# Kernel optimization log

Hardware: AMD Instinct MI355X
Metric: run time of the kernel (lower is better)

Reference implementation:

```python
import jax, jax.numpy as jnp
import numpy as np

B, S, D = 8, 2048, 1024

def setup_inputs() -> dict:
    key = jax.random.key(0)
    ks = jax.random.split(key, 7)
    x = jax.random.normal(ks[0], (B, S, D), dtype=jnp.float32)
    s = 1.0 / np.sqrt(D)
    Wq = jax.random.normal(ks[1], (D, D), dtype=jnp.float32) * s
    bq = jax.random.normal(ks[2], (D,), dtype=jnp.float32) * 0.01
    Wk = jax.random.normal(ks[3], (D, D), dtype=jnp.float32) * s
    bk = jax.random.normal(ks[4], (D,), dtype=jnp.float32) * 0.01
    Wv = jax.random.normal(ks[5], (D, D), dtype=jnp.float32) * s
    bv = jax.random.normal(ks[6], (D,), dtype=jnp.float32) * 0.01
    return {"x": x, "Wq": Wq, "bq": bq, "Wk": Wk, "bk": bk, "Wv": Wv, "bv": bv}

def reference(x, Wq, bq, Wk, bk, Wv, bv):
    # QKV projections: [B,S,D]
    Q = jnp.einsum('bsd,de->bse', x, Wq) + bq
    K = jnp.einsum('bsd,de->bse', x, Wk) + bk
    V = jnp.einsum('bsd,de->bse', x, Wv) + bv
    scale = 1.0 / jnp.sqrt(jnp.asarray(Q.shape[-1], Q.dtype))
    attn = jnp.einsum('bqd,bkd->bqk', Q, K) * scale  # [B,S,S]
    attn = jax.nn.softmax(attn, axis=-1)
    return jnp.einsum('bqk,bkd->bqd', attn, V)
```

## Files before the change

### kernel.cpp

```cpp
#include <hip/hip_runtime.h>
#include <hip/hip_bf16.h>
#include <cstdint>


#define Bb 8
#define Ss 2048
#define Dd 1024

typedef unsigned short ushort_t;
typedef __attribute__((ext_vector_type(8))) short short8;
typedef __attribute__((ext_vector_type(16))) float floatx16;

__device__ inline ushort_t f2bf(float f) {
    unsigned int u = __float_as_uint(f);
    unsigned int r = (u + 0x7fffu + ((u >> 16) & 1u)) >> 16;
    return (ushort_t)r;
}
__device__ inline float bf2f(ushort_t u) {
    return __uint_as_float(((unsigned int)u) << 16);
}

__device__ inline floatx16 mfma32(short8 a, short8 b, floatx16 c) {
    return __builtin_amdgcn_mfma_f32_32x32x16_bf16(a, b, c, 0, 0, 0);
}

__device__ inline void gload_lds16(const void* g, void* l) {
    __builtin_amdgcn_global_load_lds(
        (const __attribute__((address_space(1))) void*)g,
        (__attribute__((address_space(3))) void*)l, 16, 0, 0);
}

__device__ __attribute__((always_inline)) void gemm_core32(
    const ushort_t* __restrict__ A, const ushort_t* __restrict__ B,
    int K, int lda, int ldb, int m0, int n0, int tid,
    ushort_t* As, ushort_t* Bs, floatx16 acc[2][4])
{
    const int lane = tid & 63;
    const int wave = tid >> 6;
    const int nloc = lane & 31;
    const int h    = lane >> 5;
    const int wm   = (wave & 1) * 64;
    const int wn   = (wave >> 1) * 128;

    const int srow = lane >> 3;
    const int cg   = (lane & 7) ^ srow;
    const ushort_t* aBase = A + (size_t)(m0 + wave * 32 + srow) * lda + cg * 8;
    const ushort_t* bBase = B + (size_t)(n0 + wave * 64 + srow) * ldb + cg * 8;

    int rowA[2], rowB[4];
#pragma unroll
    for (int mt = 0; mt < 2; mt++) rowA[mt] = (wm + mt * 32 + nloc) * 64;
#pragma unroll
    for (int nt = 0; nt < 4; nt++) rowB[nt] = (wn + nt * 32 + nloc) * 64;
    const int xr = lane & 7;

    for (int kt = 0; kt < K; kt += 64) {
#pragma unroll
        for (int j = 0; j < 4; j++)
            gload_lds16(aBase + (size_t)j * 8 * lda + kt, &As[(wave * 4 + j) * 512]);
#pragma unroll
        for (int j = 0; j < 8; j++)
            gload_lds16(bBase + (size_t)j * 8 * ldb + kt, &Bs[(wave * 8 + j) * 512]);
        __syncthreads();

#pragma unroll
        for (int step = 0; step < 4; step++) {
            const int pos = (((step * 2 + h) ^ xr) * 8);
            short8 aF[2], bF[4];
#pragma unroll
            for (int mt = 0; mt < 2; mt++)
                aF[mt] = *(const short8*)&As[rowA[mt] + pos];
#pragma unroll
            for (int nt = 0; nt < 4; nt++)
                bF[nt] = *(const short8*)&Bs[rowB[nt] + pos];
#pragma unroll
            for (int mt = 0; mt < 2; mt++)
#pragma unroll
                for (int nt = 0; nt < 4; nt++)
                    acc[mt][nt] = mfma32(aF[mt], bF[nt], acc[mt][nt]);
        }
        __syncthreads();
    }
}

#define CD_ROW(reg, h) (((reg) & 3) + 8 * ((reg) >> 2) + 4 * (h))

template <int EPI>
__global__ __launch_bounds__(256, 2) void gemm_nt(
    const ushort_t* __restrict__ A, const ushort_t* __restrict__ B,
    void* __restrict__ Cv, const float* __restrict__ aux,
    int K, int lda, int ldb, int ldc,
    size_t strideA, size_t strideB, size_t strideC)
{
    const int z = blockIdx.z;
    A += (size_t)z * strideA;
    B += (size_t)z * strideB;
    const int m0 = blockIdx.y * 128;
    const int n0 = blockIdx.x * 256;

    __shared__ __align__(16) ushort_t As[128 * 64];
    __shared__ __align__(16) ushort_t Bs[256 * 64];

    const int tid  = threadIdx.x;
    const int lane = tid & 63;
    const int wave = tid >> 6;
    const int nloc = lane & 31;
    const int h    = lane >> 5;
    const int wm   = (wave & 1) * 64;
    const int wn   = (wave >> 1) * 128;

    floatx16 acc[2][4] = {};
    gemm_core32(A, B, K, lda, ldb, m0, n0, tid, As, Bs, acc);

    if (EPI == 0) {
        ushort_t* Cb = (ushort_t*)Cv;
#pragma unroll
        for (int nt = 0; nt < 4; nt++) {
            const int gc = n0 + wn + nt * 32 + nloc;
            const float bval = aux[gc];
#pragma unroll
            for (int mt = 0; mt < 2; mt++)
#pragma unroll
                for (int reg = 0; reg < 16; reg++) {
                    const int gr = m0 + wm + mt * 32 + CD_ROW(reg, h);
                    Cb[(size_t)gr * ldc + gc] = f2bf(acc[mt][nt][reg] + bval);
                }
        }
    } else {
        float* Cf = (float*)Cv + (size_t)z * strideC;
#pragma unroll
        for (int mt = 0; mt < 2; mt++)
#pragma unroll
            for (int reg = 0; reg < 16; reg++) {
                const int gr = m0 + wm + mt * 32 + CD_ROW(reg, h);
                const float iv = 1.0f / aux[z * Ss + gr];
#pragma unroll
                for (int nt = 0; nt < 4; nt++) {
                    const int gc = n0 + wn + nt * 32 + nloc;
                    Cf[(size_t)gr * ldc + gc] = acc[mt][nt][reg] * iv;
                }
            }
    }
}

__global__ __launch_bounds__(256, 2) void score_vt(
    const ushort_t* __restrict__ QKVb, ushort_t* __restrict__ Pb,
    ushort_t* __restrict__ Vt, float* __restrict__ lsum)
{
    __shared__ __align__(16) ushort_t As[128 * 64];
    __shared__ __align__(16) ushort_t Bs[256 * 64];
    const int bid = blockIdx.x;
    const int tid = threadIdx.x;

    if (bid < 1024) {
        const int nb = bid & 7, mb = (bid >> 3) & 15, z = bid >> 7;
        const int m0 = mb * 128, n0 = nb * 256;
        const ushort_t* A = QKVb + (size_t)z * Ss * 3072;
        const ushort_t* B = A + 1024;

        floatx16 acc[2][4] = {};
        gemm_core32(A, B, Dd, 3072, 3072, m0, n0, tid, As, Bs, acc);

        const int lane = tid & 63, wave = tid >> 6;
        const int nloc = lane & 31, h = lane >> 5;
        const int wm = (wave & 1) * 64, wn = (wave >> 1) * 128;
        ushort_t* Cp = Pb + (size_t)z * Ss * Ss;

        float rs[2][16] = {};
#pragma unroll
        for (int nt = 0; nt < 4; nt++) {
            const int gc = n0 + wn + nt * 32 + nloc;
#pragma unroll
            for (int mt = 0; mt < 2; mt++)
#pragma unroll
                for (int reg = 0; reg < 16; reg++) {
                    const int gr = m0 + wm + mt * 32 + CD_ROW(reg, h);
                    const ushort_t o = f2bf(__expf(acc[mt][nt][reg] * 0.03125f));
                    Cp[(size_t)gr * Ss + gc] = o;
                    rs[mt][reg] += bf2f(o);
                }
        }
#pragma unroll
        for (int mt = 0; mt < 2; mt++)
#pragma unroll
            for (int reg = 0; reg < 16; reg++) {
                float s = rs[mt][reg];
                s += __shfl_xor(s, 1);
                s += __shfl_xor(s, 2);
                s += __shfl_xor(s, 4);
                s += __shfl_xor(s, 8);
                s += __shfl_xor(s, 16);
                rs[mt][reg] = s;
            }
        if (nloc == 0) {
#pragma unroll
            for (int mt = 0; mt < 2; mt++)
#pragma unroll
                for (int reg = 0; reg < 16; reg++) {
                    const int gr = m0 + wm + mt * 32 + CD_ROW(reg, h);
                    atomicAdd(&lsum[z * Ss + gr], rs[mt][reg]);
                }
        }
    } else {
        const int t = bid - 1024;
        const int z = t >> 9, rem = t & 511;
        const int d0 = (rem & 15) * 64, s0 = (rem >> 4) * 64;
        ushort_t (*tile)[72] = (ushort_t(*)[72])As;
        const int rr = tid >> 3;
        const int c8 = (tid & 7) * 8;
#pragma unroll
        for (int i = 0; i < 2; i++) {
            const int s = s0 + rr + i * 32;
            uint4 v = *(const uint4*)&QKVb[((size_t)(z * Ss + s)) * 3072 + 2048 + d0 + c8];
            *(uint4*)&tile[rr + i * 32][c8] = v;
        }
        __syncthreads();
#pragma unroll
        for (int i = 0; i < 2; i++) {
            const int d = rr + i * 32;
            ushort_t u[8];
#pragma unroll
            for (int j = 0; j < 8; j++) u[j] = tile[c8 + j][d];
            *(uint4*)&Vt[(size_t)z * Dd * Ss + (size_t)(d0 + d) * Ss + s0 + c8] =
                *(const uint4*)u;
        }
    }
}

__global__ __launch_bounds__(256) void prep(
    const float* __restrict__ x,
    const float* __restrict__ W0, const float* __restrict__ W1,
    const float* __restrict__ W2,
    const float* __restrict__ bq, const float* __restrict__ bk,
    const float* __restrict__ bv,
    ushort_t* __restrict__ xb, ushort_t* __restrict__ Wall,
    float* __restrict__ ball)
{
    const int bid = blockIdx.x;
    const int tid = threadIdx.x;

    if (bid < 8192) {
        const size_t i = (size_t)bid * 256 + tid;
        const float4* p = (const float4*)x + i * 2;
        float4 a = p[0], b = p[1];
        ushort_t u[8];
        u[0]=f2bf(a.x); u[1]=f2bf(a.y); u[2]=f2bf(a.z); u[3]=f2bf(a.w);
        u[4]=f2bf(b.x); u[5]=f2bf(b.y); u[6]=f2bf(b.z); u[7]=f2bf(b.w);
        *(uint4*)(xb + i * 8) = *(const uint4*)u;
    } else if (bid < 8960) {
        const int t = bid - 8192;
        const int z = t >> 8;
        const float* W = (z == 0) ? W0 : (z == 1) ? W1 : W2;
        ushort_t* Wt = Wall + (size_t)z * Dd * Dd;
        __shared__ float tt[64][65];
        const int n0 = ((t >> 4) & 15) * 64, k0 = (t & 15) * 64;
        const int r  = tid >> 4;
        const int c4 = (tid & 15) * 4;
#pragma unroll
        for (int i = 0; i < 4; i++) {
            float4 v = *(const float4*)&W[(size_t)(k0 + r + i * 16) * Dd + n0 + c4];
            tt[r + i * 16][c4 + 0] = v.x;
            tt[r + i * 16][c4 + 1] = v.y;
            tt[r + i * 16][c4 + 2] = v.z;
            tt[r + i * 16][c4 + 3] = v.w;
        }
        __syncthreads();
#pragma unroll
        for (int i = 0; i < 4; i++) {
            const int rn = r + i * 16;
            ushort_t u[4];
#pragma unroll
            for (int j = 0; j < 4; j++) u[j] = f2bf(tt[c4 + j][rn]);
            *(uint2*)&Wt[(size_t)(n0 + rn) * Dd + k0 + c4] = *(const uint2*)u;
        }
    } else {
#pragma unroll
        for (int j = 0; j < 12; j++) {
            const int idx = j * 256 + tid;
            float v = (idx < 1024) ? bq[idx]
                    : (idx < 2048) ? bk[idx - 1024] : bv[idx - 2048];
            ball[idx] = v;
        }
    }
}

extern "C" void kernel_launch(void* const* d_in, const int* in_sizes, int n_in,
                              void* d_out, int out_size, void* d_ws, size_t ws_size,
                              hipStream_t stream)
{
    const float* x  = (const float*)d_in[0];
    const float* Wq = (const float*)d_in[1];
    const float* bq = (const float*)d_in[2];
    const float* Wk = (const float*)d_in[3];
    const float* bk = (const float*)d_in[4];
    const float* Wv = (const float*)d_in[5];
    const float* bv = (const float*)d_in[6];
    float* out = (float*)d_out;

    char* ws = (char*)d_ws;
    const size_t MB = 1u << 20;
    ushort_t* xb   = (ushort_t*)(ws);
    ushort_t* Vt   = (ushort_t*)(ws);
    ushort_t* QKVb = (ushort_t*)(ws + 32 * MB);
    ushort_t* Pb   = (ushort_t*)(ws + 128 * MB);
    float*    lsum = (float*)(ws + 192 * MB);
    ushort_t* Wall = (ushort_t*)d_out;
    float*    ball = (float*)((char*)d_out + 6 * MB);

    prep<<<8961, 256, 0, stream>>>(x, Wq, Wk, Wv, bq, bk, bv, xb, Wall, ball);

    dim3 g1(3072 / 256, (Bb * Ss) / 128, 1);
    gemm_nt<0><<<g1, 256, 0, stream>>>(xb, Wall, QKVb, ball,
                                       Dd, Dd, Dd, 3072, 0, 0, 0);

    hipMemsetAsync(lsum, 0, (size_t)Bb * Ss * sizeof(float), stream);
    score_vt<<<5120, 256, 0, stream>>>(QKVb, Pb, Vt, lsum);

    dim3 g3(Dd / 256, Ss / 128, Bb);
    gemm_nt<3><<<g3, 256, 0, stream>>>(Pb, Vt, out, lsum,
                                       Ss, Ss, Ss, Dd,
                                       (size_t)Ss * Ss, (size_t)Dd * Ss,
                                       (size_t)Ss * Dd);
}
```

Baseline: 421.8 us.

## Replace GEMM core with 256x256 tile, 8-wave, double-buffered 16x16 MFMA pipeline

Replaces the 128x256 single-buffered GEMM core built on 32x32 MFMA with a 256x256-tile, 512-thread kernel using 16x16x32 bf16 MFMA. The K loop is double-buffered in LDS, with global-to-LDS loads interleaved across four compute phases, explicit waitcnt/barrier scheduling and setprio. The score kernel is split out of the fused score+V-transpose launch into a separate transpose kernel plus a templated epilogue variant. Larger tiles reduce global traffic per FLOP, at the cost of 128KB LDS per block, more register pressure and a fragile hand-built pipeline.

Measured after the change: 405.2 us. 3.9% less time.

```diff
diff --git a/kernel.cpp b/kernel.cpp
--- a/kernel.cpp
+++ b/kernel.cpp
@@ -1,5 +1,4 @@
 #include <hip/hip_runtime.h>
-#include <hip/hip_bf16.h>
 #include <cstdint>
 
 
@@ -9,7 +8,7 @@
 
 typedef unsigned short ushort_t;
 typedef __attribute__((ext_vector_type(8))) short short8;
-typedef __attribute__((ext_vector_type(16))) float floatx16;
+typedef __attribute__((ext_vector_type(4))) float floatx4;
 
 __device__ inline ushort_t f2bf(float f) {
     unsigned int u = __float_as_uint(f);
@@ -20,210 +19,234 @@
     return __uint_as_float(((unsigned int)u) << 16);
 }
 
-__device__ inline floatx16 mfma32(short8 a, short8 b, floatx16 c) {
-    return __builtin_amdgcn_mfma_f32_32x32x16_bf16(a, b, c, 0, 0, 0);
-}
-
-__device__ inline void gload_lds16(const void* g, void* l) {
+__device__ inline floatx4 mfma16(short8 a, short8 b, floatx4 c) {
+    return __builtin_amdgcn_mfma_f32_16x16x32_bf16(a, b, c, 0, 0, 0);
+}
+
+__device__ inline void gload16(const void* g, void* l) {
     __builtin_amdgcn_global_load_lds(
         (const __attribute__((address_space(1))) void*)g,
         (__attribute__((address_space(3))) void*)l, 16, 0, 0);
 }
 
-__device__ __attribute__((always_inline)) void gemm_core32(
+__device__ __attribute__((always_inline)) void gemm_core256(
     const ushort_t* __restrict__ A, const ushort_t* __restrict__ B,
     int K, int lda, int ldb, int m0, int n0, int tid,
-    ushort_t* As, ushort_t* Bs, floatx16 acc[2][4])
+    ushort_t* lds, floatx4 acc[8][4])
 {
     const int lane = tid & 63;
     const int wave = tid >> 6;
-    const int nloc = lane & 31;
-    const int h    = lane >> 5;
-    const int wm   = (wave & 1) * 64;
-    const int wn   = (wave >> 1) * 128;
-
-    const int srow = lane >> 3;
-    const int cg   = (lane & 7) ^ srow;
-    const ushort_t* aBase = A + (size_t)(m0 + wave * 32 + srow) * lda + cg * 8;
-    const ushort_t* bBase = B + (size_t)(n0 + wave * 64 + srow) * ldb + cg * 8;
-
-    int rowA[2], rowB[4];
-#pragma unroll
-    for (int mt = 0; mt < 2; mt++) rowA[mt] = (wm + mt * 32 + nloc) * 64;
-#pragma unroll
-    for (int nt = 0; nt < 4; nt++) rowB[nt] = (wn + nt * 32 + nloc) * 64;
-    const int xr = lane & 7;
-
-    for (int kt = 0; kt < K; kt += 64) {
-#pragma unroll
-        for (int j = 0; j < 4; j++)
-            gload_lds16(aBase + (size_t)j * 8 * lda + kt, &As[(wave * 4 + j) * 512]);
-#pragma unroll
-        for (int j = 0; j < 8; j++)
-            gload_lds16(bBase + (size_t)j * 8 * ldb + kt, &Bs[(wave * 8 + j) * 512]);
-        __syncthreads();
-
-#pragma unroll
-        for (int step = 0; step < 4; step++) {
-            const int pos = (((step * 2 + h) ^ xr) * 8);
-            short8 aF[2], bF[4];
-#pragma unroll
-            for (int mt = 0; mt < 2; mt++)
-                aF[mt] = *(const short8*)&As[rowA[mt] + pos];
-#pragma unroll
-            for (int nt = 0; nt < 4; nt++)
-                bF[nt] = *(const short8*)&Bs[rowB[nt] + pos];
-#pragma unroll
-            for (int mt = 0; mt < 2; mt++)
-#pragma unroll
-                for (int nt = 0; nt < 4; nt++)
-                    acc[mt][nt] = mfma32(aF[mt], bF[nt], acc[mt][nt]);
-        }
-        __syncthreads();
-    }
-}
-
-#define CD_ROW(reg, h) (((reg) & 3) + 8 * ((reg) >> 2) + 4 * (h))
+    const int l3   = lane >> 3;
+    const int kc   = ((lane & 7) ^ l3) * 8;
+
+    const ushort_t* aS[2][2];
+    const ushort_t* bS[2][2];
+#pragma unroll
+    for (int i = 0; i < 2; i++) {
+#pragma unroll
+        for (int g = 0; g < 2; g++) {
+            const int r = i * 128 + g * 64 + wave * 8 + l3;
+            aS[g][i] = A + (size_t)(m0 + r) * lda + kc;
+        }
+#pragma unroll
+        for (int nh = 0; nh < 2; nh++) {
+            const int c = wave + i * 8;
+            const int r = (c >> 2) * 64 + nh * 32 + (c & 3) * 8 + l3;
+            bS[nh][i] = B + (size_t)(n0 + r) * ldb + kc;
+        }
+    }
+
+    const int jA   = (wave >> 2) * 64 + (lane & 15);
+    const int jB   = (wave & 3) * 32 + (lane & 15);
+    const int swz0 = (((lane >> 4) + 0) ^ (lane & 7)) * 8;
+    const int swz1 = (((lane >> 4) + 4) ^ (lane & 7)) * 8;
+
+#define STG(DST, REGI, SRC, KOFS)                                             \
+    do {                                                                      \
+        gload16(SRC[0] + (KOFS), (DST) + (REGI) * 8192 + wave * 512);         \
+        gload16(SRC[1] + (KOFS), (DST) + (REGI) * 8192 + (wave + 8) * 512);   \
+    } while (0)
+
+#define PHASE(MH, NH, STGSTMT, VMSTMT)                                        \
+    do {                                                                      \
+        const ushort_t* ba  = cb + (MH) * 8192;                               \
+        const ushort_t* bb2 = cb + (2 + (NH)) * 8192;                         \
+        short8 af[4][2], bf[2][2];                                            \
+        _Pragma("unroll")                                                     \
+        for (int mi = 0; mi < 4; mi++) {                                      \
+            af[mi][0] = *(const short8*)&ba[(jA + mi * 16) * 64 + swz0];      \
+            af[mi][1] = *(const short8*)&ba[(jA + mi * 16) * 64 + swz1];      \
+        }                                                                     \
+        _Pragma("unroll")                                                     \
+        for (int ni = 0; ni < 2; ni++) {                                      \
+            bf[ni][0] = *(const short8*)&bb2[(jB + ni * 16) * 64 + swz0];     \
+            bf[ni][1] = *(const short8*)&bb2[(jB + ni * 16) * 64 + swz1];     \
+        }                                                                     \
+        STGSTMT;                                                              \
+        __builtin_amdgcn_sched_barrier(0);                                    \
+        __builtin_amdgcn_s_barrier();                                         \
+        asm volatile("s_waitcnt lgkmcnt(0)" ::: "memory");                    \
+        __builtin_amdgcn_sched_barrier(0);                                    \
+        __builtin_amdgcn_s_setprio(1);                                        \
+        _Pragma("unroll")                                                     \
+        for (int ks = 0; ks < 2; ks++)                                        \
+            _Pragma("unroll")                                                 \
+            for (int mi = 0; mi < 4; mi++)                                    \
+                _Pragma("unroll")                                             \
+                for (int ni = 0; ni < 2; ni++)                                \
+                    acc[(MH) * 4 + mi][(NH) * 2 + ni] = mfma16(               \
+                        af[mi][ks], bf[ni][ks],                               \
+                        acc[(MH) * 4 + mi][(NH) * 2 + ni]);                   \
+        __builtin_amdgcn_s_setprio(0);                                        \
+        __builtin_amdgcn_sched_barrier(0);                                    \
+        VMSTMT;                                                               \
+        __builtin_amdgcn_s_barrier();                                         \
+        __builtin_amdgcn_sched_barrier(0);                                    \
+    } while (0)
+
+    STG(lds, 0, aS[0], 0);
+    STG(lds, 1, aS[1], 0);
+    STG(lds, 2, bS[0], 0);
+    STG(lds, 3, bS[1], 0);
+    STG(lds + 32768, 2, bS[0], 64);
+    STG(lds + 32768, 0, aS[0], 64);
+    asm volatile("s_waitcnt vmcnt(4)" ::: "memory");
+    __builtin_amdgcn_s_barrier();
+    __builtin_amdgcn_sched_barrier(0);
+
+    const int NT = K >> 6;
+    for (int t = 0; t < NT; t++) {
+        const ushort_t* cb = lds + (t & 1) * 32768;
+        ushort_t* nb = lds + ((t + 1) & 1) * 32768;
+        ushort_t* sb = lds + (t & 1) * 32768;
+        const int k1 = (t + 1 < NT ? t + 1 : 0) << 6;
+        const int k2 = (t + 2 < NT ? t + 2 : 0) << 6;
+        PHASE(0, 0, STG(nb, 1, aS[1], k1), (void)0);
+        PHASE(1, 0, STG(nb, 3, bS[1], k1), (void)0);
+        PHASE(0, 1, STG(sb, 2, bS[0], k2), (void)0);
+        PHASE(1, 1, STG(sb, 0, aS[0], k2),
+              asm volatile("s_waitcnt vmcnt(4)" ::: "memory"));
+    }
+    asm volatile("s_waitcnt vmcnt(0)" ::: "memory");
+#undef PHASE
+#undef STG
+}
 
 template <int EPI>
-__global__ __launch_bounds__(256, 2) void gemm_nt(
+__global__ __launch_bounds__(512, 2) void gemm256(
     const ushort_t* __restrict__ A, const ushort_t* __restrict__ B,
-    void* __restrict__ Cv, const float* __restrict__ aux,
+    void* __restrict__ Cv, float* __restrict__ aux,
     int K, int lda, int ldb, int ldc,
     size_t strideA, size_t strideB, size_t strideC)
 {
     const int z = blockIdx.z;
     A += (size_t)z * strideA;
     B += (size_t)z * strideB;
-    const int m0 = blockIdx.y * 128;
+    const int m0 = blockIdx.y * 256;
     const int n0 = blockIdx.x * 256;
 
-    __shared__ __align__(16) ushort_t As[128 * 64];
-    __shared__ __align__(16) ushort_t Bs[256 * 64];
-
-    const int tid  = threadIdx.x;
-    const int lane = tid & 63;
-    const int wave = tid >> 6;
-    const int nloc = lane & 31;
-    const int h    = lane >> 5;
-    const int wm   = (wave & 1) * 64;
-    const int wn   = (wave >> 1) * 128;
-
-    floatx16 acc[2][4] = {};
-    gemm_core32(A, B, K, lda, ldb, m0, n0, tid, As, Bs, acc);
+    __shared__ __align__(16) ushort_t lds[2 * 4 * 8192];
+
+    floatx4 acc[8][4] = {};
+    gemm_core256(A, B, K, lda, ldb, m0, n0, (int)threadIdx.x, lds, acc);
+
+    const int lane = threadIdx.x & 63;
+    const int wave = threadIdx.x >> 6;
+    const int row0 = m0 + (wave >> 2) * 128 + (lane >> 4) * 4;
+    const int col0 = n0 + (wave & 3) * 64 + (lane & 15);
 
     if (EPI == 0) {
         ushort_t* Cb = (ushort_t*)Cv;
-#pragma unroll
-        for (int nt = 0; nt < 4; nt++) {
-            const int gc = n0 + wn + nt * 32 + nloc;
-            const float bval = aux[gc];
-#pragma unroll
-            for (int mt = 0; mt < 2; mt++)
-#pragma unroll
-                for (int reg = 0; reg < 16; reg++) {
-                    const int gr = m0 + wm + mt * 32 + CD_ROW(reg, h);
-                    Cb[(size_t)gr * ldc + gc] = f2bf(acc[mt][nt][reg] + bval);
-                }
-        }
-    } else {
-        float* Cf = (float*)Cv + (size_t)z * strideC;
-#pragma unroll
-        for (int mt = 0; mt < 2; mt++)
-#pragma unroll
-            for (int reg = 0; reg < 16; reg++) {
-                const int gr = m0 + wm + mt * 32 + CD_ROW(reg, h);
-                const float iv = 1.0f / aux[z * Ss + gr];
-#pragma unroll
-                for (int nt = 0; nt < 4; nt++) {
-                    const int gc = n0 + wn + nt * 32 + nloc;
-                    Cf[(size_t)gr * ldc + gc] = acc[mt][nt][reg] * iv;
+        float bval[4];
+#pragma unroll
+        for (int nf = 0; nf < 4; nf++) bval[nf] = aux[col0 + nf * 16];
+#pragma unroll
+        for (int mf = 0; mf < 8; mf++)
+#pragma unroll
+            for (int i = 0; i < 4; i++) {
+                const size_t ro = (size_t)(row0 + mf * 16 + i) * ldc;
+#pragma unroll
+                for (int nf = 0; nf < 4; nf++)
+                    Cb[ro + col0 + nf * 16] = f2bf(acc[mf][nf][i] + bval[nf]);
+            }
+    } else if (EPI == 1) {
+        ushort_t* Cb = (ushort_t*)Cv + (size_t)z * strideC;
+        float* ls = aux + z * Ss;
+        float rs[8][4];
+#pragma unroll
+        for (int mf = 0; mf < 8; mf++)
+#pragma unroll
+            for (int i = 0; i < 4; i++) rs[mf][i] = 0.f;
+#pragma unroll
+        for (int mf = 0; mf < 8; mf++)
+#pragma unroll
+            for (int i = 0; i < 4; i++) {
+                const size_t ro = (size_t)(row0 + mf * 16 + i) * ldc;
+#pragma unroll
+                for (int nf = 0; nf < 4; nf++) {
+                    const ushort_t o = f2bf(__expf(acc[mf][nf][i] * 0.03125f));
+                    Cb[ro + col0 + nf * 16] = o;
+                    rs[mf][i] += bf2f(o);
                 }
             }
-    }
-}
-
-__global__ __launch_bounds__(256, 2) void score_vt(
-    const ushort_t* __restrict__ QKVb, ushort_t* __restrict__ Pb,
-    ushort_t* __restrict__ Vt, float* __restrict__ lsum)
-{
-    __shared__ __align__(16) ushort_t As[128 * 64];
-    __shared__ __align__(16) ushort_t Bs[256 * 64];
-    const int bid = blockIdx.x;
-    const int tid = threadIdx.x;
-
-    if (bid < 1024) {
-        const int nb = bid & 7, mb = (bid >> 3) & 15, z = bid >> 7;
-        const int m0 = mb * 128, n0 = nb * 256;
-        const ushort_t* A = QKVb + (size_t)z * Ss * 3072;
-        const ushort_t* B = A + 1024;
-
-        floatx16 acc[2][4] = {};
-        gemm_core32(A, B, Dd, 3072, 3072, m0, n0, tid, As, Bs, acc);
-
-        const int lane = tid & 63, wave = tid >> 6;
-        const int nloc = lane & 31, h = lane >> 5;
-        const int wm = (wave & 1) * 64, wn = (wave >> 1) * 128;
-        ushort_t* Cp = Pb + (size_t)z * Ss * Ss;
-
-        float rs[2][16] = {};
-#pragma unroll
-        for (int nt = 0; nt < 4; nt++) {
-            const int gc = n0 + wn + nt * 32 + nloc;
-#pragma unroll
-            for (int mt = 0; mt < 2; mt++)
-#pragma unroll
-                for (int reg = 0; reg < 16; reg++) {
-                    const int gr = m0 + wm + mt * 32 + CD_ROW(reg, h);
-                    const ushort_t o = f2bf(__expf(acc[mt][nt][reg] * 0.03125f));
-                    Cp[(size_t)gr * Ss + gc] = o;
-                    rs[mt][reg] += bf2f(o);
-                }
-        }
-#pragma unroll
-        for (int mt = 0; mt < 2; mt++)
-#pragma unroll
-            for (int reg = 0; reg < 16; reg++) {
-                float s = rs[mt][reg];
+#pragma unroll
+        for (int mf = 0; mf < 8; mf++)
+#pragma unroll
+            for (int i = 0; i < 4; i++) {
+                float s = rs[mf][i];
                 s += __shfl_xor(s, 1);
                 s += __shfl_xor(s, 2);
                 s += __shfl_xor(s, 4);
                 s += __shfl_xor(s, 8);
-                s += __shfl_xor(s, 16);
-                rs[mt][reg] = s;
+                rs[mf][i] = s;
             }
-        if (nloc == 0) {
-#pragma unroll
-            for (int mt = 0; mt < 2; mt++)
-#pragma unroll
-                for (int reg = 0; reg < 16; reg++) {
-                    const int gr = m0 + wm + mt * 32 + CD_ROW(reg, h);
-                    atomicAdd(&lsum[z * Ss + gr], rs[mt][reg]);
-                }
+        if ((lane & 15) == 0) {
+#pragma unroll
+            for (int mf = 0; mf < 8; mf++)
+#pragma unroll
+                for (int i = 0; i < 4; i++)
+                    atomicAdd(&ls[row0 + mf * 16 + i], rs[mf][i]);
         }
     } else {
-        const int t = bid - 1024;
-        const int z = t >> 9, rem = t & 511;
-        const int d0 = (rem & 15) * 64, s0 = (rem >> 4) * 64;
-        ushort_t (*tile)[72] = (ushort_t(*)[72])As;
-        const int rr = tid >> 3;
-        const int c8 = (tid & 7) * 8;
-#pragma unroll
-        for (int i = 0; i < 2; i++) {
-            const int s = s0 + rr + i * 32;
-            uint4 v = *(const uint4*)&QKVb[((size_t)(z * Ss + s)) * 3072 + 2048 + d0 + c8];
-            *(uint4*)&tile[rr + i * 32][c8] = v;
-        }
-        __syncthreads();
-#pragma unroll
-        for (int i = 0; i < 2; i++) {
-            const int d = rr + i * 32;
-            ushort_t u[8];
-#pragma unroll
-            for (int j = 0; j < 8; j++) u[j] = tile[c8 + j][d];
-            *(uint4*)&Vt[(size_t)z * Dd * Ss + (size_t)(d0 + d) * Ss + s0 + c8] =
-                *(const uint4*)u;
-        }
+        float* Cf = (float*)Cv + (size_t)z * strideC;
+#pragma unroll
+        for (int mf = 0; mf < 8; mf++)
+#pragma unroll
+            for (int i = 0; i < 4; i++) {
+                const int gr = row0 + mf * 16 + i;
+                const float iv = 1.0f / aux[z * Ss + gr];
+#pragma unroll
+                for (int nf = 0; nf < 4; nf++)
+                    Cf[(size_t)gr * ldc + col0 + nf * 16] = acc[mf][nf][i] * iv;
+            }
+    }
+}
+
+__global__ __launch_bounds__(256) void vtrans(
+    const ushort_t* __restrict__ QKVb, ushort_t* __restrict__ Vt)
+{
+    __shared__ __align__(16) ushort_t tile[64][72];
+    const int t = blockIdx.x;
+    const int z = t >> 9, rem = t & 511;
+    const int d0 = (rem & 15) * 64, s0 = (rem >> 4) * 64;
+    const int tid = threadIdx.x;
+    const int rr = tid >> 3;
+    const int c8 = (tid & 7) * 8;
+#pragma unroll
+    for (int i = 0; i < 2; i++) {
+        const int s = s0 + rr + i * 32;
+        uint4 v = *(const uint4*)&QKVb[((size_t)(z * Ss + s)) * 3072 + 2048 + d0 + c8];
+        *(uint4*)&tile[rr + i * 32][c8] = v;
+    }
+    __syncthreads();
+#pragma unroll
+    for (int i = 0; i < 2; i++) {
+        const int d = rr + i * 32;
+        ushort_t u[8];
+#pragma unroll
+        for (int j = 0; j < 8; j++) u[j] = tile[c8 + j][d];
+        *(uint4*)&Vt[(size_t)z * Dd * Ss + (size_t)(d0 + d) * Ss + s0 + c8] =
+            *(const uint4*)u;
     }
 }
 
@@ -309,15 +332,20 @@
 
     prep<<<8961, 256, 0, stream>>>(x, Wq, Wk, Wv, bq, bk, bv, xb, Wall, ball);
 
-    dim3 g1(3072 / 256, (Bb * Ss) / 128, 1);
-    gemm_nt<0><<<g1, 256, 0, stream>>>(xb, Wall, QKVb, ball,
+    dim3 g1(3072 / 256, 16384 / 256, 1);
+    gemm256<0><<<g1, 512, 0, stream>>>(xb, Wall, QKVb, ball,
                                        Dd, Dd, Dd, 3072, 0, 0, 0);
 
     hipMemsetAsync(lsum, 0, (size_t)Bb * Ss * sizeof(float), stream);
-    score_vt<<<5120, 256, 0, stream>>>(QKVb, Pb, Vt, lsum);
-
-    dim3 g3(Dd / 256, Ss / 128, Bb);
-    gemm_nt<3><<<g3, 256, 0, stream>>>(Pb, Vt, out, lsum,
+    vtrans<<<4096, 256, 0, stream>>>(QKVb, Vt);
+    dim3 g2(Ss / 256, Ss / 256, Bb);
+    gemm256<1><<<g2, 512, 0, stream>>>(QKVb, QKVb + 1024, Pb, lsum,
+                                       Dd, 3072, 3072, Ss,
+                                       (size_t)Ss * 3072, (size_t)Ss * 3072,
+                                       (size_t)Ss * Ss);
+
+    dim3 g3(Dd / 256, Ss / 256, Bb);
+    gemm256<3><<<g3, 512, 0, stream>>>(Pb, Vt, out, lsum,
                                        Ss, Ss, Ss, Dd,
                                        (size_t)Ss * Ss, (size_t)Dd * Ss,
                                        (size_t)Ss * Dd);
```
